# Optimization experiments

Measured on AMD Instinct MI355X. Metric: run time of the kernel, lower is better.

## Reference

```python
import jax, jax.numpy as jnp
import numpy as np

N, E, F, H, HEADS, L, G, NC = 50000, 800000, 128, 64, 4, 3, 64, 2
EPS = 1e-5


def _init(key, shape, fan_in):
    return jax.random.normal(key, shape, jnp.float32) / np.sqrt(fan_in)


def setup_inputs() -> dict:
    key = jax.random.key(0)
    ks = jax.random.split(key, 24)
    x = jax.random.normal(ks[0], (N, F), jnp.float32)
    edge_index = jax.random.randint(ks[1], (2, E), 0, N, jnp.int32)
    batch = jnp.sort(jax.random.randint(ks[2], (N,), 0, G, jnp.int32))
    return {
        "x": x, "edge_index": edge_index, "batch": batch,
        "Wi": _init(ks[3], (F, H), F), "bi": jnp.zeros((H,), jnp.float32),
        "gcn_W": _init(ks[4], (L, H, H), H), "gcn_b": jnp.zeros((L, H), jnp.float32),
        "gcn_gamma": jnp.ones((L, H), jnp.float32), "gcn_beta": jnp.zeros((L, H), jnp.float32),
        "Wg": _init(ks[5], (H, HEADS * H), H), "bg": jnp.zeros((H,), jnp.float32),
        "att_src": _init(ks[6], (HEADS, H), H), "att_dst": _init(ks[7], (HEADS, H), H),
        "gat_gamma": jnp.ones((H,), jnp.float32), "gat_beta": jnp.zeros((H,), jnp.float32),
        "c1_W": _init(ks[8], (2 * H, H), 2 * H), "c1_b": jnp.zeros((H,), jnp.float32),
        "c2_W": _init(ks[9], (H, H // 2), H), "c2_b": jnp.zeros((H // 2,), jnp.float32),
        "c3_W": _init(ks[10], (H // 2, NC), H // 2), "c3_b": jnp.zeros((NC,), jnp.float32),
    }


def _batch_norm(x, gamma, beta):
    # training-mode BN over the node dimension
    mu = x.mean(0)
    var = x.var(0)
    return (x - mu) * jax.lax.rsqrt(var + EPS) * gamma + beta


def _gcn_conv(x, W, b, src, dst):
    # PyG GCNConv: add self loops + symmetric normalization D^-1/2 (A+I) D^-1/2
    h = x @ W  # [N, H]
    ones = jnp.ones((src.shape[0],), h.dtype)
    deg = jax.ops.segment_sum(ones, dst, num_segments=N) + 1.0  # +1 for self loop
    dinv = jax.lax.rsqrt(deg)
    norm = dinv[src] * dinv[dst]  # [E]
    out = jax.ops.segment_sum(h[src] * norm[:, None], dst, num_segments=N)
    out = out + h * (dinv * dinv)[:, None]  # self-loop term: deg^-1
    return out + b


def _gat_conv(x, W, att_s, att_d, b, src, dst):
    # PyG GATConv, concat=False (mean over heads), leaky_relu slope 0.2, self loops
    h = (x @ W).reshape(N, HEADS, H)  # [N, Hd, C]
    a_s = (h * att_s).sum(-1)  # [N, Hd]
    a_d = (h * att_d).sum(-1)
    sl = jnp.arange(N, dtype=src.dtype)
    si = jnp.concatenate([src, sl])
    di = jnp.concatenate([dst, sl])
    logits = jax.nn.leaky_relu(a_s[si] + a_d[di], 0.2)  # [E+N, Hd]
    # segment softmax over destination node per head
    m = jax.ops.segment_max(logits, di, num_segments=N)  # every node has a self loop
    e = jnp.exp(logits - m[di])
    s = jax.ops.segment_sum(e, di, num_segments=N)
    alpha = e / (s[di] + 1e-16)  # [E+N, Hd]
    out = jax.ops.segment_sum(h[si] * alpha[:, :, None], di, num_segments=N)  # [N, Hd, C]
    return out.mean(axis=1) + b


def reference(x, edge_index, batch, Wi, bi, gcn_W, gcn_b, gcn_gamma, gcn_beta,
              Wg, bg, att_src, att_dst, gat_gamma, gat_beta,
              c1_W, c1_b, c2_W, c2_b, c3_W, c3_b):
    src, dst = edge_index[0], edge_index[1]
    h = jax.nn.relu(x @ Wi + bi)
    for l in range(L):
        identity = h
        h = _gcn_conv(h, gcn_W[l], gcn_b[l], src, dst)
        h = _batch_norm(h, gcn_gamma[l], gcn_beta[l])
        h = jax.nn.relu(h)  # dropout: eval mode (identity)
        h = h + identity
    identity = h
    h = _gat_conv(h, Wg, att_src, att_dst, bg, src, dst)
    h = _batch_norm(h, gat_gamma, gat_beta)
    h = jax.nn.elu(h)
    h = h + identity
    # dual pooling over graphs
    cnt = jax.ops.segment_sum(jnp.ones((N,), h.dtype), batch, num_segments=G,
                              indices_are_sorted=True)
    x_mean = jax.ops.segment_sum(h, batch, num_segments=G, indices_are_sorted=True)
    x_mean = x_mean / jnp.maximum(cnt, 1.0)[:, None]
    x_max = jax.ops.segment_max(h, batch, num_segments=G, indices_are_sorted=True)
    x_max = jnp.where(jnp.isfinite(x_max), x_max, 0.0)
    z = jnp.concatenate([x_mean, x_max], axis=1)  # [G, 2H]
    z = jax.nn.relu(z @ c1_W + c1_b)
    z = jax.nn.relu(z @ c2_W + c2_b)
    return z @ c3_W + c3_b  # [G, NC]
```

## Files before the change

kernel.cpp:

```cpp
#include <hip/hip_runtime.h>
#include <math.h>

#define N_ 50000
#define E_ 800000
#define F_ 128
#define H_ 64
#define G_ 64
#define NC_ 2
#define CAP_ 96
#define EPS_ 1e-5f
#define GRID_P 1250
#define WIS_STRIDE 136
#define W0_STRIDE 72
#define WGS 72

typedef _Float16 f16;
typedef f16 f16x2 __attribute__((ext_vector_type(2)));
typedef f16 f16x4 __attribute__((ext_vector_type(4)));
typedef f16 f16x8 __attribute__((ext_vector_type(8)));

__device__ __forceinline__ unsigned fkey(float f) {
    unsigned u = __float_as_uint(f);
    return (u & 0x80000000u) ? ~u : (u | 0x80000000u);
}
__device__ __forceinline__ float funkey(unsigned k) {
    unsigned u = (k & 0x80000000u) ? (k & 0x7fffffffu) : ~k;
    return __uint_as_float(u);
}
__device__ __forceinline__ float leaky(float x) { return x > 0.f ? x : 0.2f * x; }

__device__ __forceinline__ void dot8(const f16x8 w, const f16x8 v,
                                     float& a0, float& a1, float& a2, float& a3) {
    a0 = __builtin_amdgcn_fdot2(__builtin_shufflevector(w, w, 0, 1),
                                __builtin_shufflevector(v, v, 0, 1), a0, false);
    a1 = __builtin_amdgcn_fdot2(__builtin_shufflevector(w, w, 2, 3),
                                __builtin_shufflevector(v, v, 2, 3), a1, false);
    a2 = __builtin_amdgcn_fdot2(__builtin_shufflevector(w, w, 4, 5),
                                __builtin_shufflevector(v, v, 4, 5), a2, false);
    a3 = __builtin_amdgcn_fdot2(__builtin_shufflevector(w, w, 6, 7),
                                __builtin_shufflevector(v, v, 6, 7), a3, false);
}

__device__ __forceinline__ int sel4(int4 v, int i) {
    return i == 0 ? v.x : i == 1 ? v.y : i == 2 ? v.z : v.w;
}

__global__ void k_fill(const int* __restrict__ ei, int* __restrict__ rowcnt,
                       int* __restrict__ slotS) {
    int e = blockIdx.x * 256 + threadIdx.x;
    if (e >= E_) return;
    int d = ei[E_ + e];
    int pos = atomicAdd(&rowcnt[d], 1);
    if (pos < CAP_) slotS[d * CAP_ + pos] = ei[e];
}

__global__ __launch_bounds__(256) void k_in_mm(const float* __restrict__ x,
                                               const float* __restrict__ Wi,
                                               const float* __restrict__ bi,
                                               const float* __restrict__ W0,
                                               const int* __restrict__ rowcnt,
                                               float* __restrict__ hA,
                                               f16* __restrict__ hWs) {
    __shared__ __attribute__((aligned(16))) f16 Wis[H_ * WIS_STRIDE];
    __shared__ __attribute__((aligned(16))) f16 W0s[H_ * W0_STRIDE];
    __shared__ __attribute__((aligned(16))) f16 xb[4 * F_];
    __shared__ __attribute__((aligned(16))) f16 rb[4 * H_];
    int tid = threadIdx.x;
    for (int i = tid; i < F_ * H_; i += 256) {
        int k = i >> 6, j = i & 63;
        Wis[j * WIS_STRIDE + k] = (f16)Wi[i];
    }
    for (int i = tid; i < H_ * H_; i += 256) {
        int k = i >> 6, j = i & 63;
        W0s[j * W0_STRIDE + k] = (f16)W0[i];
    }
    __syncthreads();
    int r = tid >> 6, j = tid & 63;
    float bj = bi[j];
    const f16* wc1 = Wis + j * WIS_STRIDE;
    const f16* wc2 = W0s + j * W0_STRIDE;
    f16* xr = xb + r * F_;
    f16* rr = rb + r * H_;
    int grp = blockIdx.x;
    float2 xv = *(const float2*)&x[(size_t)(grp * 4 + r) * F_ + 2 * j];
    for (; grp < N_ / 4; grp += GRID_P) {
        f16x2 xs = {(f16)xv.x, (f16)xv.y};
        *(f16x2*)&xr[2 * j] = xs;
        int ng = grp + GRID_P;
        if (ng < N_ / 4)
            xv = *(const float2*)&x[(size_t)(ng * 4 + r) * F_ + 2 * j];
        int n = grp * 4 + r;
        float a0 = 0.f, a1 = 0.f, a2 = 0.f, a3 = 0.f;
#pragma unroll
        for (int k = 0; k < F_; k += 8)
            dot8(*(const f16x8*)&wc1[k], *(const f16x8*)&xr[k], a0, a1, a2, a3);
        float y = fmaxf((a0 + a1) + (a2 + a3) + bj, 0.f);
        hA[(size_t)n * H_ + j] = y;
        rr[j] = (f16)y;
        float b0 = 0.f, b1 = 0.f, b2 = 0.f, b3 = 0.f;
#pragma unroll
        for (int k = 0; k < H_; k += 8)
            dot8(*(const f16x8*)&wc2[k], *(const f16x8*)&rr[k], b0, b1, b2, b3);
        hWs[(size_t)n * H_ + j] =
            (f16)(((b0 + b1) + (b2 + b3)) * rsqrtf((float)rowcnt[n] + 1.f));
    }
}

__global__ __launch_bounds__(256) void k_gcn_gather(const int* __restrict__ rowcnt,
                                                    const int* __restrict__ slotS,
                                                    const f16* __restrict__ hWs,
                                                    float* __restrict__ out,
                                                    float* __restrict__ bnpart) {
    __shared__ float st[4][128];
    int r = threadIdx.x >> 6;
    int d = blockIdx.x * 4 + r;
    int L = threadIdx.x & 63;
    int rg = L >> 4, q = L & 15;
    int rc = rowcnt[d];
    int cnt = min(rc, CAP_);
    float dd = rsqrtf((float)rc + 1.f);
    size_t base = (size_t)d * CAP_;
    float a0 = 0.f, a1 = 0.f, a2 = 0.f, a3 = 0.f;
    if (rg == 0) {
        f16x4 hv = *(const f16x4*)&hWs[(size_t)d * H_ + q * 4];
        a0 = (float)hv[0]; a1 = (float)hv[1]; a2 = (float)hv[2]; a3 = (float)hv[3];
    }
    int k = 0;
    for (; k + 8 <= cnt; k += 8) {
        int4 sA = *(const int4*)&slotS[base + k];
        int4 sB = *(const int4*)&slotS[base + k + 4];
        int s0 = sel4(sA, rg);
        int s1 = sel4(sB, rg);
        f16x4 v0 = *(const f16x4*)&hWs[(size_t)s0 * H_ + q * 4];
        f16x4 v1 = *(const f16x4*)&hWs[(size_t)s1 * H_ + q * 4];
        a0 += (float)v0[0] + (float)v1[0];
        a1 += (float)v0[1] + (float)v1[1];
        a2 += (float)v0[2] + (float)v1[2];
        a3 += (float)v0[3] + (float)v1[3];
    }
    for (; k < cnt; k += 4) {
        if (k + rg < cnt) {
            int s = slotS[base + k + rg];
            f16x4 v = *(const f16x4*)&hWs[(size_t)s * H_ + q * 4];
            a0 += (float)v[0]; a1 += (float)v[1];
            a2 += (float)v[2]; a3 += (float)v[3];
        }
    }
    a0 += __shfl_xor(a0, 16); a0 += __shfl_xor(a0, 32);
    a1 += __shfl_xor(a1, 16); a1 += __shfl_xor(a1, 32);
    a2 += __shfl_xor(a2, 16); a2 += __shfl_xor(a2, 32);
    a3 += __shfl_xor(a3, 16); a3 += __shfl_xor(a3, 32);
    if (rg == 0) {
        float y0 = a0 * dd, y1 = a1 * dd, y2 = a2 * dd, y3 = a3 * dd;
        *(float4*)&out[(size_t)d * H_ + q * 4] = make_float4(y0, y1, y2, y3);
        st[r][q * 4 + 0] = y0;  st[r][64 + q * 4 + 0] = y0 * y0;
        st[r][q * 4 + 1] = y1;  st[r][64 + q * 4 + 1] = y1 * y1;
        st[r][q * 4 + 2] = y2;  st[r][64 + q * 4 + 2] = y2 * y2;
        st[r][q * 4 + 3] = y3;  st[r][64 + q * 4 + 3] = y3 * y3;
    }
    __syncthreads();
    for (int t = threadIdx.x; t < 128; t += 256) {
        float vsum = (st[0][t] + st[1][t]) + (st[2][t] + st[3][t]);
        atomicAdd(&bnpart[(blockIdx.x & 255) * 128 + t], vsum);
    }
}

__global__ void k_bn_final(const float* __restrict__ part, float* __restrict__ stat) {
    int t = threadIdx.x;
    float s = 0.f;
    for (int b = 0; b < 256; b++) s += part[b * 128 + t];
    __shared__ float red[128];
    red[t] = s;
    __syncthreads();
    if (t < H_) {
        float mu = red[t] / (float)N_;
        float var = red[H_ + t] / (float)N_ - mu * mu;
        stat[t] = mu;
        stat[H_ + t] = rsqrtf(var + EPS_);
    }
}

__global__ __launch_bounds__(256) void k_bn_mm(const float* __restrict__ v,
                                               const float* __restrict__ stat,
                                               const float* __restrict__ gamma,
                                               const float* __restrict__ beta,
                                               const float* __restrict__ res,
                                               const float* __restrict__ W,
                                               const int* __restrict__ rowcnt,
                                               float* __restrict__ out_res,
                                               f16* __restrict__ hWs) {
    __shared__ __attribute__((aligned(16))) f16 Ws[H_ * W0_STRIDE];
    __shared__ __attribute__((aligned(16))) f16 rb[4 * H_];
    int tid = threadIdx.x;
    for (int i = tid; i < H_ * H_; i += 256) {
        int k = i >> 6, j = i & 63;
        Ws[j * W0_STRIDE + k] = (f16)W[i];
    }
    __syncthreads();
    int r = tid >> 6, j = tid & 63;
    float mu = stat[j], rs = stat[H_ + j], ga = gamma[j], be = beta[j];
    const f16* wc = Ws + j * W0_STRIDE;
    f16* rr = rb + r * H_;
    for (int grp = blockIdx.x; grp < N_ / 4; grp += GRID_P) {
        int n = grp * 4 + r;
        size_t idx = (size_t)n * H_ + j;
        float y = (v[idx] - mu) * rs * ga + be;
        y = fmaxf(y, 0.f) + res[idx];
        out_res[idx] = y;
        rr[j] = (f16)y;
        float b0 = 0.f, b1 = 0.f, b2 = 0.f, b3 = 0.f;
#pragma unroll
        for (int k = 0; k < H_; k += 8)
            dot8(*(const f16x8*)&wc[k], *(const f16x8*)&rr[k], b0, b1, b2, b3);
        hWs[idx] = (f16)(((b0 + b1) + (b2 + b3)) * rsqrtf((float)rowcnt[n] + 1.f));
    }
}

__global__ __launch_bounds__(256) void k_wg(const float* __restrict__ v,
                                            const float* __restrict__ stat,
                                            const float* __restrict__ gamma,
                                            const float* __restrict__ beta,
                                            const float* __restrict__ res,
                                            const float* __restrict__ Wg,
                                            const float* __restrict__ asw,
                                            const float* __restrict__ adw,
                                            float* __restrict__ hOut,
                                            f16* __restrict__ hg16,
                                            float* __restrict__ a_s,
                                            float* __restrict__ a_d) {
    __shared__ __attribute__((aligned(16))) f16 Wgs[256 * WGS];
    __shared__ __attribute__((aligned(16))) f16 xb[32 * H_];
    int tid = threadIdx.x;
    for (int i = tid; i < H_ * 256; i += 256) {
        int k = i >> 8, j = i & 255;
        Wgs[j * WGS + k] = (f16)Wg[i];
    }
    int n0 = blockIdx.x * 32;
    int nrows = min(32, N_ - n0);
    {
        int c = tid & 63;
        float mu = stat[c], rs = stat[H_ + c], ga = gamma[c], be = beta[c];
        for (int i = tid; i < nrows * H_; i += 256) {
            size_t idx = (size_t)n0 * H_ + i;
            float y = (v[idx] - mu) * rs * ga + be;
            y = fmaxf(y, 0.f) + res[idx];
            hOut[idx] = y;
            xb[i] = (f16)y;
        }
    }
    __syncthreads();
    int j = tid, wid = j >> 6, lane = j & 63;
    float aw = asw[j], dw = adw[j];
    const f16* wcol = &Wgs[j * WGS];
    for (int nn = 0; nn < nrows; nn++) {
        const f16* hr = xb + nn * H_;
        float a0 = 0.f, a1 = 0.f, a2 = 0.f, a3 = 0.f;
#pragma unroll
        for (int k = 0; k < H_; k += 8)
            dot8(*(const f16x8*)&wcol[k], *(const f16x8*)&hr[k], a0, a1, a2, a3);
        float acc = (a0 + a1) + (a2 + a3);
        int n = n0 + nn;
        hg16[(size_t)n * 256 + j] = (f16)acc;
        float ps = acc * aw, pd = acc * dw;
        for (int m = 1; m < 64; m <<= 1) {
            ps += __shfl_xor(ps, m);
            pd += __shfl_xor(pd, m);
        }
        if (lane == 0) { a_s[n * 4 + wid] = ps; a_d[n * 4 + wid] = pd; }
    }
}

__global__ __launch_bounds__(256) void k_gat(const int* __restrict__ rowcnt,
                                             const int* __restrict__ slotS,
                                             const f16* __restrict__ hg16,
                                             const float* __restrict__ a_s,
                                             const float* __restrict__ a_d,
                                             float* __restrict__ out,
                                             float* __restrict__ bnpart) {
    __shared__ float st[4][128];
    int r = threadIdx.x >> 6;
    int d = blockIdx.x * 4 + r;
    int L = threadIdx.x & 63;
    int rg = L >> 5, p = L & 31;
    int h = p >> 3, o = p & 7;
    int cnt = min(rowcnt[d], CAP_);
    size_t base = (size_t)d * CAP_;
    float ads = a_d[d * 4 + h];
    float es = __expf(fminf(leaky(a_s[d * 4 + h] + ads), 19.f) - 8.f);
    float s = 0.f;
    float acc[8];
#pragma unroll
    for (int i = 0; i < 8; i++) acc[i] = 0.f;
    if (rg == 0) {
        s = es;
        f16x8 hv = *(const f16x8*)&hg16[(size_t)d * 256 + p * 8];
#pragma unroll
        for (int i = 0; i < 8; i++) acc[i] = es * (float)hv[i];
    }
    int k = 0;
    for (; k + 8 <= cnt; k += 8) {
        int4 sA = *(const int4*)&slotS[base + k];
        int4 sB = *(const int4*)&slotS[base + k + 4];
        int s0 = rg ? sA.y : sA.x;
        int s1 = rg ? sA.w : sA.z;
        int s2 = rg ? sB.y : sB.x;
        int s3 = rg ? sB.w : sB.z;
        float x0 = a_s[s0 * 4 + h];
        float x1 = a_s[s1 * 4 + h];
        float x2 = a_s[s2 * 4 + h];
        float x3 = a_s[s3 * 4 + h];
        f16x8 v0 = *(const f16x8*)&hg16[(size_t)s0 * 256 + p * 8];
        f16x8 v1 = *(const f16x8*)&hg16[(size_t)s1 * 256 + p * 8];
        f16x8 v2 = *(const f16x8*)&hg16[(size_t)s2 * 256 + p * 8];
        f16x8 v3 = *(const f16x8*)&hg16[(size_t)s3 * 256 + p * 8];
        float t0 = __expf(fminf(leaky(x0 + ads), 19.f) - 8.f);
        float t1 = __expf(fminf(leaky(x1 + ads), 19.f) - 8.f);
        float t2 = __expf(fminf(leaky(x2 + ads), 19.f) - 8.f);
        float t3 = __expf(fminf(leaky(x3 + ads), 19.f) - 8.f);
        s += (t0 + t1) + (t2 + t3);
#pragma unroll
        for (int i = 0; i < 8; i++)
            acc[i] += (t0 * (float)v0[i] + t1 * (float)v1[i]) +
                      (t2 * (float)v2[i] + t3 * (float)v3[i]);
    }
    for (; k < cnt; k += 2) {
        if (k + rg < cnt) {
            int sE = slotS[base + k + rg];
            float t = __expf(fminf(leaky(a_s[sE * 4 + h] + ads), 19.f) - 8.f);
            f16x8 v = *(const f16x8*)&hg16[(size_t)sE * 256 + p * 8];
            s += t;
#pragma unroll
            for (int i = 0; i < 8; i++) acc[i] += t * (float)v[i];
        }
    }
    s += __shfl_xor(s, 32);
#pragma unroll
    for (int i = 0; i < 8; i++) acc[i] += __shfl_xor(acc[i], 32);
    float w = 0.25f / (s + 1e-16f);
#pragma unroll
    for (int i = 0; i < 8; i++) acc[i] *= w;
#pragma unroll
    for (int i = 0; i < 8; i++) {
        acc[i] += __shfl_xor(acc[i], 8);
        acc[i] += __shfl_xor(acc[i], 16);
    }
    if (L < 8) {
        float4 oA = make_float4(acc[0], acc[1], acc[2], acc[3]);
        float4 oB = make_float4(acc[4], acc[5], acc[6], acc[7]);
        *(float4*)&out[(size_t)d * H_ + o * 8] = oA;
        *(float4*)&out[(size_t)d * H_ + o * 8 + 4] = oB;
#pragma unroll
        for (int i = 0; i < 8; i++) {
            st[r][o * 8 + i] = acc[i];
            st[r][64 + o * 8 + i] = acc[i] * acc[i];
        }
    }
    __syncthreads();
    for (int t = threadIdx.x; t < 128; t += 256) {
        float vsum = (st[0][t] + st[1][t]) + (st[2][t] + st[3][t]);
        atomicAdd(&bnpart[(blockIdx.x & 255) * 128 + t], vsum);
    }
}

__global__ __launch_bounds__(256) void k_pool_bn(const float* __restrict__ accv,
                                                 const float* __restrict__ stat,
                                                 const float* __restrict__ gamma,
                                                 const float* __restrict__ beta,
                                                 const float* __restrict__ res,
                                                 const int* __restrict__ batch,
                                                 float* __restrict__ xmean,
                                                 unsigned int* __restrict__ xmaxb,
                                                 float* __restrict__ cnt) {
    const int CH = 196;
    int n0 = blockIdx.x * CH;
    int nEnd = min(n0 + CH, N_);
    int c = threadIdx.x & 63, r = threadIdx.x >> 6;
    float mu = stat[c], rs = stat[H_ + c], ga = gamma[c], be = beta[c];
    int curg = -1, cc = 0;
    float s = 0.f;
    unsigned mk = 0u;
    for (int n = n0 + r; n < nEnd; n += 4) {
        int g = batch[n];
        if (g != curg) {
            if (curg >= 0) {
                atomicAdd(&xmean[curg * H_ + c], s);
                atomicMax(&xmaxb[curg * H_ + c], mk);
                if (c == 0) atomicAdd(&cnt[curg], (float)cc);
            }
            curg = g; s = 0.f; mk = 0u; cc = 0;
        }
        size_t idx = (size_t)n * H_ + c;
        float y = (accv[idx] - mu) * rs * ga + be;
        y = (y > 0.f ? y : expf(y) - 1.f) + res[idx];
        s += y;
        unsigned kv = fkey(y);
        mk = mk > kv ? mk : kv;
        cc++;
    }
    if (curg >= 0) {
        atomicAdd(&xmean[curg * H_ + c], s);
        atomicMax(&xmaxb[curg * H_ + c], mk);
        if (c == 0) atomicAdd(&cnt[curg], (float)cc);
    }
}

__global__ __launch_bounds__(64) void k_head(const float* __restrict__ xmean,
                                             const unsigned int* __restrict__ xmaxb,
                                             const float* __restrict__ cnt,
                                             const float* __restrict__ c1W, const float* __restrict__ c1b,
                                             const float* __restrict__ c2W, const float* __restrict__ c2b,
                                             const float* __restrict__ c3W, const float* __restrict__ c3b,
                                             float* __restrict__ out) {
    __shared__ float z[2 * H_];
    __shared__ float o1[H_];
    __shared__ float o2[32];
    int g = blockIdx.x, j = threadIdx.x;
    float cn = fmaxf(cnt[g], 1.f);
    z[j] = xmean[g * H_ + j] / cn;
    unsigned key = xmaxb[g * H_ + j];
    z[H_ + j] = (key == 0u) ? 0.f : funkey(key);
    __syncthreads();
    float a0 = c1b[j], a1 = 0.f, a2 = 0.f, a3 = 0.f;
    for (int k = 0; k < 2 * H_; k += 4) {
        a0 += z[k] * c1W[k * 64 + j];
        a1 += z[k + 1] * c1W[(k + 1) * 64 + j];
        a2 += z[k + 2] * c1W[(k + 2) * 64 + j];
        a3 += z[k + 3] * c1W[(k + 3) * 64 + j];
    }
    o1[j] = fmaxf((a0 + a1) + (a2 + a3), 0.f);
    __syncthreads();
    if (j < 32) {
        float b0 = c2b[j], b1 = 0.f, b2 = 0.f, b3 = 0.f;
        for (int k = 0; k < H_; k += 4) {
            b0 += o1[k] * c2W[k * 32 + j];
            b1 += o1[k + 1] * c2W[(k + 1) * 32 + j];
            b2 += o1[k + 2] * c2W[(k + 2) * 32 + j];
            b3 += o1[k + 3] * c2W[(k + 3) * 32 + j];
        }
        o2[j] = fmaxf((b0 + b1) + (b2 + b3), 0.f);
    }
    __syncthreads();
    if (j < NC_) {
        float c0 = c3b[j];
        for (int k = 0; k < 32; k++) c0 += o2[k] * c3W[k * 2 + j];
        out[g * NC_ + j] = c0;
    }
}

extern "C" void kernel_launch(void* const* d_in, const int* in_sizes, int n_in,
                              void* d_out, int out_size, void* d_ws, size_t ws_size,
                              hipStream_t stream) {
    const float* x     = (const float*)d_in[0];
    const int*   ei    = (const int*)d_in[1];
    const int*   batch = (const int*)d_in[2];
    const float* Wi    = (const float*)d_in[3];
    const float* bi    = (const float*)d_in[4];
    const float* gcnW  = (const float*)d_in[5];
    const float* gcnG  = (const float*)d_in[7];
    const float* gcnB  = (const float*)d_in[8];
    const float* Wg    = (const float*)d_in[9];
    const float* attS  = (const float*)d_in[11];
    const float* attD  = (const float*)d_in[12];
    const float* gatG  = (const float*)d_in[13];
    const float* gatB  = (const float*)d_in[14];
    const float* c1W   = (const float*)d_in[15];
    const float* c1b   = (const float*)d_in[16];
    const float* c2W   = (const float*)d_in[17];
    const float* c2b   = (const float*)d_in[18];
    const float* c3W   = (const float*)d_in[19];
    const float* c3b   = (const float*)d_in[20];
    float* out = (float*)d_out;

    float* p = (float*)d_ws;
    float* hA    = p; p += (size_t)N_ * H_;
    float* hB    = p; p += (size_t)N_ * H_;
    float* acc   = p; p += (size_t)N_ * H_;
    f16*   hg16  = (f16*)p; p += (size_t)N_ * 128;
    float* a_s   = p; p += (size_t)N_ * 4;
    float* a_d   = p; p += (size_t)N_ * 4;
    float* bnstat = p; p += 2 * H_;
    float* xmean  = p; p += G_ * H_;
    unsigned int* xmaxb = (unsigned int*)p; p += G_ * H_;
    float* cnt = p; p += G_;
    int* rowcnt = (int*)p; p += N_;
    float* bnpart4 = p; p += 4 * 256 * 128;
    int* slotS = (int*)p; p += (size_t)N_ * CAP_ + 16;
    f16* hWs = (f16*)hg16;

    float* bnp0 = bnpart4;
    float* bnp1 = bnpart4 + 1 * 256 * 128;
    float* bnp2 = bnpart4 + 2 * 256 * 128;
    float* bnp3 = bnpart4 + 3 * 256 * 128;

    const int NB_E = (E_ + 255) / 256;
    const int NB_W = N_ / 4;

    hipMemsetAsync(rowcnt, 0, (N_ + 4 * 256 * 128) * sizeof(float), stream);
    k_fill<<<NB_E, 256, 0, stream>>>(ei, rowcnt, slotS);

    k_in_mm<<<GRID_P, 256, 0, stream>>>(x, Wi, bi, gcnW, rowcnt, hA, hWs);

    k_gcn_gather<<<NB_W, 256, 0, stream>>>(rowcnt, slotS, hWs, acc, bnp0);
    k_bn_final<<<1, 128, 0, stream>>>(bnp0, bnstat);
    k_bn_mm<<<GRID_P, 256, 0, stream>>>(acc, bnstat, gcnG, gcnB, hA,
                                        gcnW + (size_t)1 * H_ * H_, rowcnt, hB, hWs);
    k_gcn_gather<<<NB_W, 256, 0, stream>>>(rowcnt, slotS, hWs, acc, bnp1);
    k_bn_final<<<1, 128, 0, stream>>>(bnp1, bnstat);
    k_bn_mm<<<GRID_P, 256, 0, stream>>>(acc, bnstat, gcnG + H_, gcnB + H_, hB,
                                        gcnW + (size_t)2 * H_ * H_, rowcnt, hA, hWs);
    k_gcn_gather<<<NB_W, 256, 0, stream>>>(rowcnt, slotS, hWs, acc, bnp2);
    k_bn_final<<<1, 128, 0, stream>>>(bnp2, bnstat);

    k_wg<<<(N_ + 31) / 32, 256, 0, stream>>>(acc, bnstat, gcnG + 2 * H_, gcnB + 2 * H_,
                                             hA, Wg, attS, attD, hB, hg16, a_s, a_d);
    k_gat<<<NB_W, 256, 0, stream>>>(rowcnt, slotS, hg16, a_s, a_d, acc, bnp3);
    k_bn_final<<<1, 128, 0, stream>>>(bnp3, bnstat);

    hipMemsetAsync(xmean, 0, (G_ * H_ * 2 + G_) * sizeof(float), stream);
    k_pool_bn<<<256, 256, 0, stream>>>(acc, bnstat, gatG, gatB, hB, batch,
                                       xmean, xmaxb, cnt);

    k_head<<<G_, 64, 0, stream>>>(xmean, xmaxb, cnt, c1W, c1b, c2W, c2b, c3W, c3b, out);
}
```

Baseline: 480.1 us.

## Slice GAT features per head-half and gather edges lane-parallel with atomic output

k_wg now writes the GAT features as 8 separate slices of 32 halfs per node, one per head and half-channel, instead of one 256-wide row per node. k_gat launches one block per (16 destination nodes, slice), with 16 edges processed in parallel per wavefront, and combines the heads into the output with atomicAdd into a zeroed buffer. The aim is a smaller, more local gather footprint per pass and more memory-level parallelism per node. In exchange, edge indices and attention scores are re-read once per slice, and every output element takes four atomics. BatchNorm statistics move out of k_gat into a new k_bn_stats kernel that makes an extra full read of the output.

```diff
diff --git a/kernel.cpp b/kernel.cpp
--- a/kernel.cpp
+++ b/kernel.cpp
@@ -165,6 +165,26 @@
     }
 }
 
+__global__ __launch_bounds__(256) void k_bn_stats(const float* __restrict__ v,
+                                                  float* __restrict__ part) {
+    __shared__ float ss[H_], sq[H_];
+    if (threadIdx.x < H_) { ss[threadIdx.x] = 0.f; sq[threadIdx.x] = 0.f; }
+    __syncthreads();
+    int c = threadIdx.x & 63;
+    float ls = 0.f, lq = 0.f;
+    for (int idx = blockIdx.x * 256 + threadIdx.x; idx < N_ * H_; idx += 256 * 256) {
+        float val = v[idx];
+        ls += val; lq += val * val;
+    }
+    atomicAdd(&ss[c], ls);
+    atomicAdd(&sq[c], lq);
+    __syncthreads();
+    if (threadIdx.x < H_) {
+        part[blockIdx.x * 128 + threadIdx.x] = ss[threadIdx.x];
+        part[blockIdx.x * 128 + H_ + threadIdx.x] = sq[threadIdx.x];
+    }
+}
+
 __global__ void k_bn_final(const float* __restrict__ part, float* __restrict__ stat) {
     int t = threadIdx.x;
     float s = 0.f;
@@ -252,6 +272,7 @@
     int j = tid, wid = j >> 6, lane = j & 63;
     float aw = asw[j], dw = adw[j];
     const f16* wcol = &Wgs[j * WGS];
+    size_t slbase = (size_t)(j >> 5) * ((size_t)N_ * 32) + (j & 31);
     for (int nn = 0; nn < nrows; nn++) {
         const f16* hr = xb + nn * H_;
         float a0 = 0.f, a1 = 0.f, a2 = 0.f, a3 = 0.f;
@@ -260,7 +281,7 @@
             dot8(*(const f16x8*)&wcol[k], *(const f16x8*)&hr[k], a0, a1, a2, a3);
         float acc = (a0 + a1) + (a2 + a3);
         int n = n0 + nn;
-        hg16[(size_t)n * 256 + j] = (f16)acc;
+        hg16[slbase + (size_t)n * 32] = (f16)acc;
         float ps = acc * aw, pd = acc * dw;
         for (int m = 1; m < 64; m <<= 1) {
             ps += __shfl_xor(ps, m);
@@ -270,19 +291,19 @@
     }
 }
 
-__global__ __launch_bounds__(256) void k_gat(const int* __restrict__ rowcnt,
-                                             const int* __restrict__ slotS,
-                                             const f16* __restrict__ hg16,
-                                             const float* __restrict__ a_s,
-                                             const float* __restrict__ a_d,
-                                             float* __restrict__ out,
-                                             float* __restrict__ bnpart) {
-    __shared__ float st[4][128];
-    int r = threadIdx.x >> 6;
-    int d = blockIdx.x * 4 + r;
+__global__ __launch_bounds__(1024) void k_gat(const int* __restrict__ rowcnt,
+                                              const int* __restrict__ slotS,
+                                              const f16* __restrict__ hgs,
+                                              const float* __restrict__ a_s,
+                                              const float* __restrict__ a_d,
+                                              float* __restrict__ out) {
+    int j = blockIdx.x & 7;
+    int dg = blockIdx.x >> 3;
+    int d = dg * 16 + (threadIdx.x >> 6);
     int L = threadIdx.x & 63;
-    int rg = L >> 5, p = L & 31;
-    int h = p >> 3, o = p & 7;
+    int eg = L >> 2, q = L & 3;
+    int h = j >> 1;
+    const f16* hsl = hgs + (size_t)j * ((size_t)N_ * 32);
     int cnt = min(rowcnt[d], CAP_);
     size_t base = (size_t)d * CAP_;
     float ads = a_d[d * 4 + h];
@@ -291,74 +312,34 @@
     float acc[8];
 #pragma unroll
     for (int i = 0; i < 8; i++) acc[i] = 0.f;
-    if (rg == 0) {
+    if (eg == 0) {
         s = es;
-        f16x8 hv = *(const f16x8*)&hg16[(size_t)d * 256 + p * 8];
+        f16x8 hv = *(const f16x8*)&hsl[(size_t)d * 32 + q * 8];
 #pragma unroll
         for (int i = 0; i < 8; i++) acc[i] = es * (float)hv[i];
     }
-    int k = 0;
-    for (; k + 8 <= cnt; k += 8) {
-        int4 sA = *(const int4*)&slotS[base + k];
-        int4 sB = *(const int4*)&slotS[base + k + 4];
-        int s0 = rg ? sA.y : sA.x;
-        int s1 = rg ? sA.w : sA.z;
-        int s2 = rg ? sB.y : sB.x;
-        int s3 = rg ? sB.w : sB.z;
-        float x0 = a_s[s0 * 4 + h];
-        float x1 = a_s[s1 * 4 + h];
-        float x2 = a_s[s2 * 4 + h];
-        float x3 = a_s[s3 * 4 + h];
-        f16x8 v0 = *(const f16x8*)&hg16[(size_t)s0 * 256 + p * 8];
-        f16x8 v1 = *(const f16x8*)&hg16[(size_t)s1 * 256 + p * 8];
-        f16x8 v2 = *(const f16x8*)&hg16[(size_t)s2 * 256 + p * 8];
-        f16x8 v3 = *(const f16x8*)&hg16[(size_t)s3 * 256 + p * 8];
-        float t0 = __expf(fminf(leaky(x0 + ads), 19.f) - 8.f);
-        float t1 = __expf(fminf(leaky(x1 + ads), 19.f) - 8.f);
-        float t2 = __expf(fminf(leaky(x2 + ads), 19.f) - 8.f);
-        float t3 = __expf(fminf(leaky(x3 + ads), 19.f) - 8.f);
-        s += (t0 + t1) + (t2 + t3);
-#pragma unroll
-        for (int i = 0; i < 8; i++)
-            acc[i] += (t0 * (float)v0[i] + t1 * (float)v1[i]) +
-                      (t2 * (float)v2[i] + t3 * (float)v3[i]);
-    }
-    for (; k < cnt; k += 2) {
-        if (k + rg < cnt) {
-            int sE = slotS[base + k + rg];
-            float t = __expf(fminf(leaky(a_s[sE * 4 + h] + ads), 19.f) - 8.f);
-            f16x8 v = *(const f16x8*)&hg16[(size_t)sE * 256 + p * 8];
-            s += t;
-#pragma unroll
-            for (int i = 0; i < 8; i++) acc[i] += t * (float)v[i];
-        }
-    }
-    s += __shfl_xor(s, 32);
-#pragma unroll
-    for (int i = 0; i < 8; i++) acc[i] += __shfl_xor(acc[i], 32);
-    float w = 0.25f / (s + 1e-16f);
-#pragma unroll
-    for (int i = 0; i < 8; i++) acc[i] *= w;
-#pragma unroll
-    for (int i = 0; i < 8; i++) {
-        acc[i] += __shfl_xor(acc[i], 8);
-        acc[i] += __shfl_xor(acc[i], 16);
-    }
-    if (L < 8) {
-        float4 oA = make_float4(acc[0], acc[1], acc[2], acc[3]);
-        float4 oB = make_float4(acc[4], acc[5], acc[6], acc[7]);
-        *(float4*)&out[(size_t)d * H_ + o * 8] = oA;
-        *(float4*)&out[(size_t)d * H_ + o * 8 + 4] = oB;
-#pragma unroll
-        for (int i = 0; i < 8; i++) {
-            st[r][o * 8 + i] = acc[i];
-            st[r][64 + o * 8 + i] = acc[i] * acc[i];
-        }
-    }
-    __syncthreads();
-    for (int t = threadIdx.x; t < 128; t += 256) {
-        float vsum = (st[0][t] + st[1][t]) + (st[2][t] + st[3][t]);
-        atomicAdd(&bnpart[(blockIdx.x & 255) * 128 + t], vsum);
+    for (int k = 0; k < cnt; k += 16) {
+        int e = k + eg;
+        int slot = slotS[base + e];
+        bool act = e < cnt;
+        int se = act ? slot : d;
+        float xa = a_s[se * 4 + h];
+        f16x8 hv = *(const f16x8*)&hsl[(size_t)se * 32 + q * 8];
+        float t = act ? __expf(fminf(leaky(xa + ads), 19.f) - 8.f) : 0.f;
+        s += t;
+#pragma unroll
+        for (int i = 0; i < 8; i++) acc[i] += t * (float)hv[i];
+    }
+#pragma unroll
+    for (int m = 4; m <= 32; m <<= 1) {
+        s += __shfl_xor(s, m);
+#pragma unroll
+        for (int i = 0; i < 8; i++) acc[i] += __shfl_xor(acc[i], m);
+    }
+    float wgt = 0.25f / (s + 1e-16f);
+    if (L < 32) {
+        int i = L >> 2;
+        atomicAdd(&out[(size_t)d * H_ + (j & 1) * 32 + q * 8 + i], wgt * acc[i]);
     }
 }
 
@@ -513,7 +494,9 @@
 
     k_wg<<<(N_ + 31) / 32, 256, 0, stream>>>(acc, bnstat, gcnG + 2 * H_, gcnB + 2 * H_,
                                              hA, Wg, attS, attD, hB, hg16, a_s, a_d);
-    k_gat<<<NB_W, 256, 0, stream>>>(rowcnt, slotS, hg16, a_s, a_d, acc, bnp3);
+    hipMemsetAsync(acc, 0, (size_t)N_ * H_ * sizeof(float), stream);
+    k_gat<<<(N_ / 16) * 8, 1024, 0, stream>>>(rowcnt, slotS, hg16, a_s, a_d, acc);
+    k_bn_stats<<<256, 256, 0, stream>>>(acc, bnp3);
     k_bn_final<<<1, 128, 0, stream>>>(bnp3, bnstat);
 
     hipMemsetAsync(xmean, 0, (G_ * H_ * 2 + G_) * sizeof(float), stream);
```

New measurement: 622.3 us. 29.6% more time.

## Split GCN feature table into column halves and compress neighbor indices to u16

Applied to the files above, without the earlier changes.

The fp16 transformed-feature table is stored as two separate 32-column halves, and the GCN gather launches twice as many blocks, each handling one half. Each half-table is small enough to have a better chance of staying resident in cache during the random neighbor gathers. Neighbor slot indices are stored as 16-bit values, which halves index traffic in the GCN and GAT gathers; this depends on N fitting in 16 bits. In exchange, each index list is read twice, once per half, and the BN partial sums are written per half.

```diff
diff --git a/kernel.cpp b/kernel.cpp
--- a/kernel.cpp
+++ b/kernel.cpp
@@ -13,11 +13,14 @@
 #define WIS_STRIDE 136
 #define W0_STRIDE 72
 #define WGS 72
+#define N32 (N_ * 32)
 
 typedef _Float16 f16;
 typedef f16 f16x2 __attribute__((ext_vector_type(2)));
 typedef f16 f16x4 __attribute__((ext_vector_type(4)));
 typedef f16 f16x8 __attribute__((ext_vector_type(8)));
+typedef unsigned short u16;
+typedef u16 u16x8 __attribute__((ext_vector_type(8)));
 
 __device__ __forceinline__ unsigned fkey(float f) {
     unsigned u = __float_as_uint(f);
@@ -41,17 +44,13 @@
                                 __builtin_shufflevector(v, v, 6, 7), a3, false);
 }
 
-__device__ __forceinline__ int sel4(int4 v, int i) {
-    return i == 0 ? v.x : i == 1 ? v.y : i == 2 ? v.z : v.w;
-}
-
 __global__ void k_fill(const int* __restrict__ ei, int* __restrict__ rowcnt,
-                       int* __restrict__ slotS) {
+                       u16* __restrict__ slotS) {
     int e = blockIdx.x * 256 + threadIdx.x;
     if (e >= E_) return;
     int d = ei[E_ + e];
     int pos = atomicAdd(&rowcnt[d], 1);
-    if (pos < CAP_) slotS[d * CAP_ + pos] = ei[e];
+    if (pos < CAP_) slotS[d * CAP_ + pos] = (u16)ei[e];
 }
 
 __global__ __launch_bounds__(256) void k_in_mm(const float* __restrict__ x,
@@ -81,6 +80,7 @@
     const f16* wc2 = W0s + j * W0_STRIDE;
     f16* xr = xb + r * F_;
     f16* rr = rb + r * H_;
+    size_t wsoff = (size_t)(j >> 5) * N32 + (j & 31);
     int grp = blockIdx.x;
     float2 xv = *(const float2*)&x[(size_t)(grp * 4 + r) * F_ + 2 * j];
     for (; grp < N_ / 4; grp += GRID_P) {
@@ -101,67 +101,66 @@
 #pragma unroll
         for (int k = 0; k < H_; k += 8)
             dot8(*(const f16x8*)&wc2[k], *(const f16x8*)&rr[k], b0, b1, b2, b3);
-        hWs[(size_t)n * H_ + j] =
+        hWs[wsoff + (size_t)n * 32] =
             (f16)(((b0 + b1) + (b2 + b3)) * rsqrtf((float)rowcnt[n] + 1.f));
     }
 }
 
 __global__ __launch_bounds__(256) void k_gcn_gather(const int* __restrict__ rowcnt,
-                                                    const int* __restrict__ slotS,
+                                                    const u16* __restrict__ slotS,
                                                     const f16* __restrict__ hWs,
                                                     float* __restrict__ out,
                                                     float* __restrict__ bnpart) {
     __shared__ float st[4][128];
+    int sl = blockIdx.x & 1;
     int r = threadIdx.x >> 6;
-    int d = blockIdx.x * 4 + r;
+    int d = (blockIdx.x >> 1) * 4 + r;
     int L = threadIdx.x & 63;
-    int rg = L >> 4, q = L & 15;
+    int rg = L >> 3, q = L & 7;
     int rc = rowcnt[d];
     int cnt = min(rc, CAP_);
     float dd = rsqrtf((float)rc + 1.f);
     size_t base = (size_t)d * CAP_;
+    const f16* tab = hWs + (size_t)sl * N32;
     float a0 = 0.f, a1 = 0.f, a2 = 0.f, a3 = 0.f;
     if (rg == 0) {
-        f16x4 hv = *(const f16x4*)&hWs[(size_t)d * H_ + q * 4];
+        f16x4 hv = *(const f16x4*)&tab[(size_t)d * 32 + q * 4];
         a0 = (float)hv[0]; a1 = (float)hv[1]; a2 = (float)hv[2]; a3 = (float)hv[3];
     }
-    int k = 0;
-    for (; k + 8 <= cnt; k += 8) {
-        int4 sA = *(const int4*)&slotS[base + k];
-        int4 sB = *(const int4*)&slotS[base + k + 4];
-        int s0 = sel4(sA, rg);
-        int s1 = sel4(sB, rg);
-        f16x4 v0 = *(const f16x4*)&hWs[(size_t)s0 * H_ + q * 4];
-        f16x4 v1 = *(const f16x4*)&hWs[(size_t)s1 * H_ + q * 4];
-        a0 += (float)v0[0] + (float)v1[0];
-        a1 += (float)v0[1] + (float)v1[1];
-        a2 += (float)v0[2] + (float)v1[2];
-        a3 += (float)v0[3] + (float)v1[3];
-    }
-    for (; k < cnt; k += 4) {
-        if (k + rg < cnt) {
-            int s = slotS[base + k + rg];
-            f16x4 v = *(const f16x4*)&hWs[(size_t)s * H_ + q * 4];
-            a0 += (float)v[0]; a1 += (float)v[1];
-            a2 += (float)v[2]; a3 += (float)v[3];
-        }
-    }
-    a0 += __shfl_xor(a0, 16); a0 += __shfl_xor(a0, 32);
-    a1 += __shfl_xor(a1, 16); a1 += __shfl_xor(a1, 32);
-    a2 += __shfl_xor(a2, 16); a2 += __shfl_xor(a2, 32);
-    a3 += __shfl_xor(a3, 16); a3 += __shfl_xor(a3, 32);
+    for (int k = 0; k < cnt; k += 16) {
+        u16x8 iA = *(const u16x8*)&slotS[base + k];
+        u16x8 iB = *(const u16x8*)&slotS[base + k + 8];
+        int e0 = k + rg, e1 = k + 8 + rg;
+        int s0 = (e0 < cnt) ? (int)iA[rg] : d;
+        int s1 = (e1 < cnt) ? (int)iB[rg] : d;
+        f16x4 v0 = *(const f16x4*)&tab[(size_t)s0 * 32 + q * 4];
+        f16x4 v1 = *(const f16x4*)&tab[(size_t)s1 * 32 + q * 4];
+        float m0 = (e0 < cnt) ? 1.f : 0.f;
+        float m1 = (e1 < cnt) ? 1.f : 0.f;
+        a0 += m0 * (float)v0[0] + m1 * (float)v1[0];
+        a1 += m0 * (float)v0[1] + m1 * (float)v1[1];
+        a2 += m0 * (float)v0[2] + m1 * (float)v1[2];
+        a3 += m0 * (float)v0[3] + m1 * (float)v1[3];
+    }
+    a0 += __shfl_xor(a0, 8); a0 += __shfl_xor(a0, 16); a0 += __shfl_xor(a0, 32);
+    a1 += __shfl_xor(a1, 8); a1 += __shfl_xor(a1, 16); a1 += __shfl_xor(a1, 32);
+    a2 += __shfl_xor(a2, 8); a2 += __shfl_xor(a2, 16); a2 += __shfl_xor(a2, 32);
+    a3 += __shfl_xor(a3, 8); a3 += __shfl_xor(a3, 16); a3 += __shfl_xor(a3, 32);
     if (rg == 0) {
         float y0 = a0 * dd, y1 = a1 * dd, y2 = a2 * dd, y3 = a3 * dd;
-        *(float4*)&out[(size_t)d * H_ + q * 4] = make_float4(y0, y1, y2, y3);
-        st[r][q * 4 + 0] = y0;  st[r][64 + q * 4 + 0] = y0 * y0;
-        st[r][q * 4 + 1] = y1;  st[r][64 + q * 4 + 1] = y1 * y1;
-        st[r][q * 4 + 2] = y2;  st[r][64 + q * 4 + 2] = y2 * y2;
-        st[r][q * 4 + 3] = y3;  st[r][64 + q * 4 + 3] = y3 * y3;
-    }
-    __syncthreads();
-    for (int t = threadIdx.x; t < 128; t += 256) {
-        float vsum = (st[0][t] + st[1][t]) + (st[2][t] + st[3][t]);
-        atomicAdd(&bnpart[(blockIdx.x & 255) * 128 + t], vsum);
+        *(float4*)&out[(size_t)d * H_ + sl * 32 + q * 4] = make_float4(y0, y1, y2, y3);
+        int c = sl * 32 + q * 4;
+        st[r][c + 0] = y0;  st[r][64 + c + 0] = y0 * y0;
+        st[r][c + 1] = y1;  st[r][64 + c + 1] = y1 * y1;
+        st[r][c + 2] = y2;  st[r][64 + c + 2] = y2 * y2;
+        st[r][c + 3] = y3;  st[r][64 + c + 3] = y3 * y3;
+    }
+    __syncthreads();
+    if (threadIdx.x < 64) {
+        int t = threadIdx.x;
+        int c = sl * 32 + (t & 31) + (t >> 5) * 64;
+        float vsum = (st[0][c] + st[1][c]) + (st[2][c] + st[3][c]);
+        atomicAdd(&bnpart[(blockIdx.x & 255) * 128 + c], vsum);
     }
 }
 
@@ -201,6 +200,7 @@
     float mu = stat[j], rs = stat[H_ + j], ga = gamma[j], be = beta[j];
     const f16* wc = Ws + j * W0_STRIDE;
     f16* rr = rb + r * H_;
+    size_t wsoff = (size_t)(j >> 5) * N32 + (j & 31);
     for (int grp = blockIdx.x; grp < N_ / 4; grp += GRID_P) {
         int n = grp * 4 + r;
         size_t idx = (size_t)n * H_ + j;
@@ -212,7 +212,8 @@
 #pragma unroll
         for (int k = 0; k < H_; k += 8)
             dot8(*(const f16x8*)&wc[k], *(const f16x8*)&rr[k], b0, b1, b2, b3);
-        hWs[idx] = (f16)(((b0 + b1) + (b2 + b3)) * rsqrtf((float)rowcnt[n] + 1.f));
+        hWs[wsoff + (size_t)n * 32] =
+            (f16)(((b0 + b1) + (b2 + b3)) * rsqrtf((float)rowcnt[n] + 1.f));
     }
 }
 
@@ -271,7 +272,7 @@
 }
 
 __global__ __launch_bounds__(256) void k_gat(const int* __restrict__ rowcnt,
-                                             const int* __restrict__ slotS,
+                                             const u16* __restrict__ slotS,
                                              const f16* __restrict__ hg16,
                                              const float* __restrict__ a_s,
                                              const float* __restrict__ a_d,
@@ -299,12 +300,11 @@
     }
     int k = 0;
     for (; k + 8 <= cnt; k += 8) {
-        int4 sA = *(const int4*)&slotS[base + k];
-        int4 sB = *(const int4*)&slotS[base + k + 4];
-        int s0 = rg ? sA.y : sA.x;
-        int s1 = rg ? sA.w : sA.z;
-        int s2 = rg ? sB.y : sB.x;
-        int s3 = rg ? sB.w : sB.z;
+        u16x8 iA = *(const u16x8*)&slotS[base + k];
+        int s0 = (int)iA[rg];
+        int s1 = (int)iA[2 + rg];
+        int s2 = (int)iA[4 + rg];
+        int s3 = (int)iA[6 + rg];
         float x0 = a_s[s0 * 4 + h];
         float x1 = a_s[s1 * 4 + h];
         float x2 = a_s[s2 * 4 + h];
@@ -325,7 +325,7 @@
     }
     for (; k < cnt; k += 2) {
         if (k + rg < cnt) {
-            int sE = slotS[base + k + rg];
+            int sE = (int)slotS[base + k + rg];
             float t = __expf(fminf(leaky(a_s[sE * 4 + h] + ads), 19.f) - 8.f);
             f16x8 v = *(const f16x8*)&hg16[(size_t)sE * 256 + p * 8];
             s += t;
@@ -484,7 +484,7 @@
     float* cnt = p; p += G_;
     int* rowcnt = (int*)p; p += N_;
     float* bnpart4 = p; p += 4 * 256 * 128;
-    int* slotS = (int*)p; p += (size_t)N_ * CAP_ + 16;
+    u16* slotS = (u16*)p; p += (size_t)N_ * CAP_ / 2 + 8;
     f16* hWs = (f16*)hg16;
 
     float* bnp0 = bnpart4;
@@ -494,21 +494,22 @@
 
     const int NB_E = (E_ + 255) / 256;
     const int NB_W = N_ / 4;
+    const int NB_G = NB_W * 2;
 
     hipMemsetAsync(rowcnt, 0, (N_ + 4 * 256 * 128) * sizeof(float), stream);
     k_fill<<<NB_E, 256, 0, stream>>>(ei, rowcnt, slotS);
 
     k_in_mm<<<GRID_P, 256, 0, stream>>>(x, Wi, bi, gcnW, rowcnt, hA, hWs);
 
-    k_gcn_gather<<<NB_W, 256, 0, stream>>>(rowcnt, slotS, hWs, acc, bnp0);
+    k_gcn_gather<<<NB_G, 256, 0, stream>>>(rowcnt, slotS, hWs, acc, bnp0);
     k_bn_final<<<1, 128, 0, stream>>>(bnp0, bnstat);
     k_bn_mm<<<GRID_P, 256, 0, stream>>>(acc, bnstat, gcnG, gcnB, hA,
                                         gcnW + (size_t)1 * H_ * H_, rowcnt, hB, hWs);
-    k_gcn_gather<<<NB_W, 256, 0, stream>>>(rowcnt, slotS, hWs, acc, bnp1);
+    k_gcn_gather<<<NB_G, 256, 0, stream>>>(rowcnt, slotS, hWs, acc, bnp1);
     k_bn_final<<<1, 128, 0, stream>>>(bnp1, bnstat);
     k_bn_mm<<<GRID_P, 256, 0, stream>>>(acc, bnstat, gcnG + H_, gcnB + H_, hB,
                                         gcnW + (size_t)2 * H_ * H_, rowcnt, hA, hWs);
-    k_gcn_gather<<<NB_W, 256, 0, stream>>>(rowcnt, slotS, hWs, acc, bnp2);
+    k_gcn_gather<<<NB_G, 256, 0, stream>>>(rowcnt, slotS, hWs, acc, bnp2);
     k_bn_final<<<1, 128, 0, stream>>>(bnp2, bnstat);
 
     k_wg<<<(N_ + 31) / 32, 256, 0, stream>>>(acc, bnstat, gcnG + 2 * H_, gcnB + 2 * H_,
```

Measured after the change: 491.0 us. 2.3% more time.

## Store neighbor slot indices as 16-bit and unroll GCN gather to 4 loads

Applied to the files above, without the earlier changes.

Neighbor slot indices are compacted from int32 to uint16 (N=50000 fits), which halves the index-table traffic in the fill, GCN gather and GAT kernels. The GCN gather loop is restructured into a single masked loop that issues four row loads per iteration with out-of-range lanes redirected to the node's own row and zeroed by a mask. The workspace is reordered so one memset clears the counters, BN partials and pooling buffers, removing a second memset launch. The narrowing depends on node ids staying below 65536, and the masked loop does some wasted loads on short rows.

```diff
diff --git a/kernel.cpp b/kernel.cpp
--- a/kernel.cpp
+++ b/kernel.cpp
@@ -18,6 +18,8 @@
 typedef f16 f16x2 __attribute__((ext_vector_type(2)));
 typedef f16 f16x4 __attribute__((ext_vector_type(4)));
 typedef f16 f16x8 __attribute__((ext_vector_type(8)));
+typedef unsigned short u16;
+typedef u16 u16x8 __attribute__((ext_vector_type(8)));
 
 __device__ __forceinline__ unsigned fkey(float f) {
     unsigned u = __float_as_uint(f);
@@ -41,17 +43,13 @@
                                 __builtin_shufflevector(v, v, 6, 7), a3, false);
 }
 
-__device__ __forceinline__ int sel4(int4 v, int i) {
-    return i == 0 ? v.x : i == 1 ? v.y : i == 2 ? v.z : v.w;
-}
-
 __global__ void k_fill(const int* __restrict__ ei, int* __restrict__ rowcnt,
-                       int* __restrict__ slotS) {
+                       u16* __restrict__ slotS) {
     int e = blockIdx.x * 256 + threadIdx.x;
     if (e >= E_) return;
     int d = ei[E_ + e];
     int pos = atomicAdd(&rowcnt[d], 1);
-    if (pos < CAP_) slotS[d * CAP_ + pos] = ei[e];
+    if (pos < CAP_) slotS[d * CAP_ + pos] = (u16)ei[e];
 }
 
 __global__ __launch_bounds__(256) void k_in_mm(const float* __restrict__ x,
@@ -107,7 +105,7 @@
 }
 
 __global__ __launch_bounds__(256) void k_gcn_gather(const int* __restrict__ rowcnt,
-                                                    const int* __restrict__ slotS,
+                                                    const u16* __restrict__ slotS,
                                                     const f16* __restrict__ hWs,
                                                     float* __restrict__ out,
                                                     float* __restrict__ bnpart) {
@@ -125,26 +123,30 @@
         f16x4 hv = *(const f16x4*)&hWs[(size_t)d * H_ + q * 4];
         a0 = (float)hv[0]; a1 = (float)hv[1]; a2 = (float)hv[2]; a3 = (float)hv[3];
     }
-    int k = 0;
-    for (; k + 8 <= cnt; k += 8) {
-        int4 sA = *(const int4*)&slotS[base + k];
-        int4 sB = *(const int4*)&slotS[base + k + 4];
-        int s0 = sel4(sA, rg);
-        int s1 = sel4(sB, rg);
+    for (int k = 0; k < cnt; k += 16) {
+        u16x8 iA = *(const u16x8*)&slotS[base + k];
+        u16x8 iB = *(const u16x8*)&slotS[base + k + 8];
+        int e = k + rg;
+        int s0 = (e < cnt) ? (int)iA[rg] : d;
+        int s1 = (e + 4 < cnt) ? (int)iA[4 + rg] : d;
+        int s2 = (e + 8 < cnt) ? (int)iB[rg] : d;
+        int s3 = (e + 12 < cnt) ? (int)iB[4 + rg] : d;
         f16x4 v0 = *(const f16x4*)&hWs[(size_t)s0 * H_ + q * 4];
         f16x4 v1 = *(const f16x4*)&hWs[(size_t)s1 * H_ + q * 4];
-        a0 += (float)v0[0] + (float)v1[0];
-        a1 += (float)v0[1] + (float)v1[1];
-        a2 += (float)v0[2] + (float)v1[2];
-        a3 += (float)v0[3] + (float)v1[3];
-    }
-    for (; k < cnt; k += 4) {
-        if (k + rg < cnt) {
-            int s = slotS[base + k + rg];
-            f16x4 v = *(const f16x4*)&hWs[(size_t)s * H_ + q * 4];
-            a0 += (float)v[0]; a1 += (float)v[1];
-            a2 += (float)v[2]; a3 += (float)v[3];
-        }
+        f16x4 v2 = *(const f16x4*)&hWs[(size_t)s2 * H_ + q * 4];
+        f16x4 v3 = *(const f16x4*)&hWs[(size_t)s3 * H_ + q * 4];
+        float m0 = (e < cnt) ? 1.f : 0.f;
+        float m1 = (e + 4 < cnt) ? 1.f : 0.f;
+        float m2 = (e + 8 < cnt) ? 1.f : 0.f;
+        float m3 = (e + 12 < cnt) ? 1.f : 0.f;
+        a0 += (m0 * (float)v0[0] + m1 * (float)v1[0]) +
+              (m2 * (float)v2[0] + m3 * (float)v3[0]);
+        a1 += (m0 * (float)v0[1] + m1 * (float)v1[1]) +
+              (m2 * (float)v2[1] + m3 * (float)v3[1]);
+        a2 += (m0 * (float)v0[2] + m1 * (float)v1[2]) +
+              (m2 * (float)v2[2] + m3 * (float)v3[2]);
+        a3 += (m0 * (float)v0[3] + m1 * (float)v1[3]) +
+              (m2 * (float)v2[3] + m3 * (float)v3[3]);
     }
     a0 += __shfl_xor(a0, 16); a0 += __shfl_xor(a0, 32);
     a1 += __shfl_xor(a1, 16); a1 += __shfl_xor(a1, 32);
@@ -271,7 +273,7 @@
 }
 
 __global__ __launch_bounds__(256) void k_gat(const int* __restrict__ rowcnt,
-                                             const int* __restrict__ slotS,
+                                             const u16* __restrict__ slotS,
                                              const f16* __restrict__ hg16,
                                              const float* __restrict__ a_s,
                                              const float* __restrict__ a_d,
@@ -299,12 +301,11 @@
     }
     int k = 0;
     for (; k + 8 <= cnt; k += 8) {
-        int4 sA = *(const int4*)&slotS[base + k];
-        int4 sB = *(const int4*)&slotS[base + k + 4];
-        int s0 = rg ? sA.y : sA.x;
-        int s1 = rg ? sA.w : sA.z;
-        int s2 = rg ? sB.y : sB.x;
-        int s3 = rg ? sB.w : sB.z;
+        u16x8 iA = *(const u16x8*)&slotS[base + k];
+        int s0 = (int)iA[rg];
+        int s1 = (int)iA[2 + rg];
+        int s2 = (int)iA[4 + rg];
+        int s3 = (int)iA[6 + rg];
         float x0 = a_s[s0 * 4 + h];
         float x1 = a_s[s1 * 4 + h];
         float x2 = a_s[s2 * 4 + h];
@@ -325,7 +326,7 @@
     }
     for (; k < cnt; k += 2) {
         if (k + rg < cnt) {
-            int sE = slotS[base + k + rg];
+            int sE = (int)slotS[base + k + rg];
             float t = __expf(fminf(leaky(a_s[sE * 4 + h] + ads), 19.f) - 8.f);
             f16x8 v = *(const f16x8*)&hg16[(size_t)sE * 256 + p * 8];
             s += t;
@@ -479,12 +480,13 @@
     float* a_s   = p; p += (size_t)N_ * 4;
     float* a_d   = p; p += (size_t)N_ * 4;
     float* bnstat = p; p += 2 * H_;
+    int* rowcnt = (int*)p; p += N_;
+    float* bnpart4 = p; p += 4 * 256 * 128;
     float* xmean  = p; p += G_ * H_;
     unsigned int* xmaxb = (unsigned int*)p; p += G_ * H_;
     float* cnt = p; p += G_;
-    int* rowcnt = (int*)p; p += N_;
-    float* bnpart4 = p; p += 4 * 256 * 128;
-    int* slotS = (int*)p; p += (size_t)N_ * CAP_ + 16;
+    const size_t ZWORDS = (size_t)N_ + 4 * 256 * 128 + G_ * H_ * 2 + G_;
+    u16* slotS = (u16*)p; p += (size_t)N_ * CAP_ / 2 + 8;
     f16* hWs = (f16*)hg16;
 
     float* bnp0 = bnpart4;
@@ -495,7 +497,7 @@
     const int NB_E = (E_ + 255) / 256;
     const int NB_W = N_ / 4;
 
-    hipMemsetAsync(rowcnt, 0, (N_ + 4 * 256 * 128) * sizeof(float), stream);
+    hipMemsetAsync(rowcnt, 0, ZWORDS * sizeof(float), stream);
     k_fill<<<NB_E, 256, 0, stream>>>(ei, rowcnt, slotS);
 
     k_in_mm<<<GRID_P, 256, 0, stream>>>(x, Wi, bi, gcnW, rowcnt, hA, hWs);
@@ -516,7 +518,6 @@
     k_gat<<<NB_W, 256, 0, stream>>>(rowcnt, slotS, hg16, a_s, a_d, acc, bnp3);
     k_bn_final<<<1, 128, 0, stream>>>(bnp3, bnstat);
 
-    hipMemsetAsync(xmean, 0, (G_ * H_ * 2 + G_) * sizeof(float), stream);
     k_pool_bn<<<256, 256, 0, stream>>>(acc, bnstat, gatG, gatB, hB, batch,
                                        xmean, xmaxb, cnt);
 
```

After: 452.3 us. -5.8%, faster.
